# Optimization experiments

Measured on AMD Instinct MI355X. Metric: run time of the kernel, lower is better.

Reference implementation:

```python
import jax, jax.numpy as jnp
import numpy as np

QLEN, BSZ, D_MODEL = 2048, 4, 1024
N_HEAD, D_HEAD = 16, 64
SCALE = 1.0 / D_HEAD ** 0.5


def _rope(t, cos, sin):
    # t: [len, b, n, d_head]; cos/sin: [len, d_head//2]
    tr = t.reshape(*t.shape[:-1], D_HEAD // 2, 2)
    t_r, t_i = tr[..., 0], tr[..., 1]
    c = cos[:, None, None, :]
    s = sin[:, None, None, :]
    o_r = t_r * c - t_i * s
    o_i = t_r * s + t_i * c
    return jnp.stack([o_r, o_i], axis=-1).reshape(t.shape)


def setup_inputs() -> dict:
    key = jax.random.key(0)
    ks = jax.random.split(key, 9)
    x = jax.random.normal(ks[0], (QLEN, BSZ, D_MODEL), dtype=jnp.float32)
    # standard RoPE frequencies: theta = 10000^{-2i/d_head}
    inv_freq = 1.0 / (10000.0 ** (np.arange(0, D_HEAD, 2, dtype=np.float32) / D_HEAD))
    ang = np.arange(QLEN, dtype=np.float32)[:, None] * inv_freq[None, :]
    freqs_cos = jnp.asarray(np.cos(ang))
    freqs_sin = jnp.asarray(np.sin(ang))
    init = lambda k, sh: (jax.random.normal(k, sh, dtype=jnp.float32) * 0.02)
    H = N_HEAD * D_HEAD
    return {
        "x": x,
        "freqs_cos": freqs_cos,
        "freqs_sin": freqs_sin,
        "Wq": init(ks[1], (D_MODEL, H)), "bq": jnp.zeros((H,), jnp.float32),
        "Wk": init(ks[2], (D_MODEL, H)), "bk": jnp.zeros((H,), jnp.float32),
        "Wv": init(ks[3], (D_MODEL, H)), "bv": jnp.zeros((H,), jnp.float32),
        "Wo": init(ks[4], (H, D_MODEL)), "bo": jnp.zeros((D_MODEL,), jnp.float32),
    }


def reference(x, freqs_cos, freqs_sin, Wq, bq, Wk, bk, Wv, bv, Wo, bo):
    qlen, bsz, _ = x.shape
    q = x @ Wq + bq  # [q, b, n*d]
    k = x @ Wk + bk
    v = x @ Wv + bv
    new_mem = (k, v)
    q = q.reshape(qlen, bsz, N_HEAD, D_HEAD)
    k = k.reshape(qlen, bsz, N_HEAD, D_HEAD)
    vv = v.reshape(qlen, bsz, N_HEAD, D_HEAD)
    q = _rope(q, freqs_cos, freqs_sin)
    k = _rope(k, freqs_cos, freqs_sin)
    attn = jnp.einsum('ibnd,jbnd->ijbn', q, k) * SCALE
    p = jax.nn.softmax(attn, axis=1)
    o = jnp.einsum('ijbn,jbnd->ibnd', p, vv)
    o = o.reshape(qlen, bsz, N_HEAD * D_HEAD) @ Wo + bo
    return (o, new_mem[0], new_mem[1])
```

## Files before the change

### kernel.cpp

```cpp
#include <hip/hip_runtime.h>

typedef __attribute__((ext_vector_type(4))) float f32x4;
typedef __attribute__((ext_vector_type(16))) float f32x16;
typedef __attribute__((ext_vector_type(8))) __bf16 bf16x8;
typedef __attribute__((ext_vector_type(4))) __bf16 bf16x4;
typedef __attribute__((ext_vector_type(2))) __bf16 bf16x2;
typedef __attribute__((ext_vector_type(4))) unsigned int u32x4;

#define DEVI __device__ __forceinline__

static constexpr int QLEN = 2048, BSZ = 4, DM = 1024, NH = 16, DH = 64;
static constexpr int MROWS = QLEN * BSZ;
static constexpr long OSZ  = (long)MROWS * DM;
static constexpr float SCL2E = 0.125f * 1.4426950408889634f;
static constexpr float RAW_THR = 4.0f / SCL2E;

DEVI void gload_lds16(const void* g, void* l) {
  __builtin_amdgcn_global_load_lds(
      (__attribute__((address_space(1))) void*)(size_t)g,
      (__attribute__((address_space(3))) void*)l, 16, 0, 0);
}

DEVI f32x16 zero16() {
  f32x16 v;
#pragma unroll
  for (int i = 0; i < 16; ++i) v[i] = 0.f;
  return v;
}

DEVI unsigned pack_bf16(float lo, float hi) {
  bf16x2 v = { (__bf16)lo, (__bf16)hi };
  return __builtin_bit_cast(unsigned, v);
}

__global__ void k_f32_to_bf16(const float* __restrict__ in, __bf16* __restrict__ out, int n4) {
  int i = blockIdx.x * blockDim.x + threadIdx.x;
  int stride = gridDim.x * blockDim.x;
  for (; i < n4; i += stride) {
    const float4 v = ((const float4*)in)[i];
    bf16x4 o = { (__bf16)v.x, (__bf16)v.y, (__bf16)v.z, (__bf16)v.w };
    ((bf16x4*)out)[i] = o;
  }
}

__global__ void k_wtrans(const float* __restrict__ W, __bf16* __restrict__ Wt) {
  __shared__ float tile[64][65];
  const int tk = blockIdx.x >> 4;
  const int tn = blockIdx.x & 15;
  const int t = threadIdx.x;
  const int r = t >> 4;
  const int c4 = (t & 15) << 2;
#pragma unroll
  for (int i = 0; i < 4; ++i) {
    const float4 v = *(const float4*)&W[(size_t)(tk * 64 + r + i * 16) * DM + tn * 64 + c4];
    tile[r + i * 16][c4 + 0] = v.x;
    tile[r + i * 16][c4 + 1] = v.y;
    tile[r + i * 16][c4 + 2] = v.z;
    tile[r + i * 16][c4 + 3] = v.w;
  }
  __syncthreads();
#pragma unroll
  for (int i = 0; i < 4; ++i) {
    const int n = r + i * 16;
    bf16x4 o = { (__bf16)tile[c4 + 0][n], (__bf16)tile[c4 + 1][n],
                 (__bf16)tile[c4 + 2][n], (__bf16)tile[c4 + 3][n] };
    *(bf16x4*)&Wt[(size_t)(tn * 64 + n) * DM + tk * 64 + c4] = o;
  }
}

__global__ __launch_bounds__(256, 4) void k_vtrans(const __bf16* __restrict__ vb,
                                                   __bf16* __restrict__ VT) {
  __shared__ __bf16 tile[128 * 72];
  const int t = threadIdx.x;
  const int bh = blockIdx.x >> 4;
  const int s0 = (blockIdx.x & 15) * 128;
  const int b = bh >> 4, h = bh & 15;

  {
    const int r = t >> 1, hh = t & 1;
    const __bf16* src = vb + (size_t)((s0 + r) * 4 + b) * DM + h * 64 + hh * 32;
    __bf16* dst = tile + r * 72 + hh * 32;
#pragma unroll
    for (int k = 0; k < 4; ++k)
      *(bf16x8*)(dst + k * 8) = *(const bf16x8*)(src + k * 8);
  }
  __syncthreads();

  const int l = t & 63;
  const int w = t >> 6;
  const int hf = l >> 5;
#pragma unroll
  for (int gi = 0; gi < 4; ++gi) {
    const int idx = w * 4 + gi;
    const int ktl = idx >> 3;
    const int fi = idx & 7;
    const int jc = fi >> 1, dh = fi & 1;
    const int d = dh * 32 + (l & 31);
    const int j8 = ktl * 64 + jc * 16 + hf * 8;
    bf16x8 pk;
#pragma unroll
    for (int jj = 0; jj < 8; ++jj) pk[jj] = tile[(j8 + jj) * 72 + d];
    const int kt_g = (blockIdx.x & 15) * 2 + ktl;
    *(bf16x8*)&VT[(size_t)(((bh * 32 + kt_g) * 8 + fi) * 64 + l) * 8] = pk;
  }
}

DEVI void gemm_tile_core(const __bf16* __restrict__ A, const __bf16* __restrict__ Bt,
                         char* Alds, char* Blds, int m0, int n0, int t,
                         f32x4 (&acc)[4][4]) {
  constexpr int K = 1024;
  const int l = t & 63;
  const int w = t >> 6;
  const int wr = w >> 1, wc = w & 1;

  int a_addr[2][4], b_addr[2][4];
#pragma unroll
  for (int s = 0; s < 2; ++s)
#pragma unroll
    for (int f = 0; f < 4; ++f) {
      const int ca = s * 64 + ((l >> 4) << 4);
      const int ra = wr * 64 + f * 16 + (l & 15);
      a_addr[s][f] = ra * 128 + (ca ^ ((ra & 7) << 4));
      const int rb = wc * 64 + f * 16 + (l & 15);
      b_addr[s][f] = rb * 128 + (ca ^ ((rb & 7) << 4));
    }

  int g_row[4], g_col[4];
#pragma unroll
  for (int i = 0; i < 4; ++i) {
    const int g = i * 256 + t;
    g_row[i] = g >> 3;
    g_col[i] = ((g & 7) ^ (g_row[i] & 7)) * 8;
  }

  for (int kt = 0; kt < K / 64; ++kt) {
#pragma unroll
    for (int i = 0; i < 4; ++i) {
      gload_lds16(A + (size_t)(m0 + g_row[i]) * K + kt * 64 + g_col[i],
                  Alds + (size_t)(i * 256 + t) * 16);
      gload_lds16(Bt + (size_t)(n0 + g_row[i]) * K + kt * 64 + g_col[i],
                  Blds + (size_t)(i * 256 + t) * 16);
    }
    __syncthreads();
#pragma unroll
    for (int s = 0; s < 2; ++s) {
      bf16x8 af[4], bfr[4];
#pragma unroll
      for (int f = 0; f < 4; ++f) {
        af[f]  = *(const bf16x8*)(Alds + a_addr[s][f]);
        bfr[f] = *(const bf16x8*)(Blds + b_addr[s][f]);
      }
      __builtin_amdgcn_s_setprio(1);
#pragma unroll
      for (int mi = 0; mi < 4; ++mi)
#pragma unroll
        for (int ni = 0; ni < 4; ++ni)
          acc[mi][ni] = __builtin_amdgcn_mfma_f32_16x16x32_bf16(af[mi], bfr[ni], acc[mi][ni], 0, 0, 0);
      __builtin_amdgcn_s_setprio(0);
    }
    __syncthreads();
  }
}

__global__ __launch_bounds__(256, 2) void k_gemm(
    const __bf16* __restrict__ A, const __bf16* __restrict__ Bt,
    const float* __restrict__ bias, float* __restrict__ Cf) {
  __shared__ alignas(16) char lds[32768];
  const int t = threadIdx.x;
  const int l = t & 63;
  const int w = t >> 6;
  const int n0 = (blockIdx.x & 7) * 128;
  const int m0 = (blockIdx.x >> 3) * 128;
  const int wr = w >> 1, wc = w & 1;

  f32x4 acc[4][4];
#pragma unroll
  for (int i = 0; i < 4; ++i)
#pragma unroll
    for (int j = 0; j < 4; ++j) acc[i][j] = (f32x4){0.f, 0.f, 0.f, 0.f};

  gemm_tile_core(A, Bt, lds, lds + 16384, m0, n0, t, acc);

  const int rowb = m0 + wr * 64 + ((l >> 4) << 2);
  const int colb = n0 + wc * 64 + (l & 15);
#pragma unroll
  for (int ni = 0; ni < 4; ++ni) {
    const float bv = bias[colb + ni * 16];
#pragma unroll
    for (int mi = 0; mi < 4; ++mi)
#pragma unroll
      for (int r = 0; r < 4; ++r)
        Cf[(size_t)(rowb + mi * 16 + r) * 1024 + colb + ni * 16] = acc[mi][ni][r] + bv;
  }
}

__global__ __launch_bounds__(256, 2) void k_gemm_qkv(
    const __bf16* __restrict__ A, const __bf16* __restrict__ Bt,
    const float* __restrict__ bq, const float* __restrict__ bk, const float* __restrict__ bv,
    const float* __restrict__ fc, const float* __restrict__ fs,
    float* __restrict__ ok, float* __restrict__ ov,
    __bf16* __restrict__ qr, __bf16* __restrict__ kr, __bf16* __restrict__ vb) {
  __shared__ alignas(16) char lds[32768];
  const int t = threadIdx.x;
  const int l = t & 63;
  const int w = t >> 6;
  const int nt = blockIdx.x % 24;
  const int n0 = nt * 128;
  const int m0 = (blockIdx.x / 24) * 128;
  const int wr = w >> 1, wc = w & 1;

  f32x4 acc[4][4];
#pragma unroll
  for (int i = 0; i < 4; ++i)
#pragma unroll
    for (int j = 0; j < 4; ++j) acc[i][j] = (f32x4){0.f, 0.f, 0.f, 0.f};

  gemm_tile_core(A, Bt, lds, lds + 16384, m0, n0, t, acc);

  const int grp = n0 >> 10;
  const int rowb = m0 + wr * 64 + ((l >> 4) << 2);
  const int colb = (n0 & 1023) + wc * 64 + (l & 15);

  if (grp == 2) {
#pragma unroll
    for (int ni = 0; ni < 4; ++ni) {
      const float bvv = bv[colb + ni * 16];
#pragma unroll
      for (int mi = 0; mi < 4; ++mi)
#pragma unroll
        for (int r = 0; r < 4; ++r) {
          const float v = acc[mi][ni][r] + bvv;
          const size_t idx = (size_t)(rowb + mi * 16 + r) * 1024 + colb + ni * 16;
          ov[idx] = v;
          vb[idx] = (__bf16)v;
        }
    }
  } else {
    const float* bias = grp == 0 ? bq : bk;
    __bf16* Rb = grp == 0 ? qr : kr;
    const float sgn = (l & 1) ? 1.f : -1.f;
#pragma unroll
    for (int ni = 0; ni < 4; ++ni) {
      const int col = colb + ni * 16;
      const float bvv = bias[col];
      const int p = (col & 63) >> 1;
#pragma unroll
      for (int mi = 0; mi < 4; ++mi) {
        const int s_idx = (rowb + mi * 16) >> 2;
        const float cv = fc[s_idx * 32 + p];
        const float sv = fs[s_idx * 32 + p] * sgn;
#pragma unroll
        for (int r = 0; r < 4; ++r) {
          const float v = acc[mi][ni][r] + bvv;
          if (grp == 1) ok[(size_t)(rowb + mi * 16 + r) * 1024 + col] = v;
          const float part = __shfl_xor(v, 1);
          Rb[(size_t)(rowb + mi * 16 + r) * 1024 + col] = (__bf16)(v * cv + part * sv);
        }
      }
    }
  }
}

static constexpr int FBUF5 = 16384;

__global__ __launch_bounds__(256, 4) void k_flash5(
    const __bf16* __restrict__ Q, const __bf16* __restrict__ Kr,
    const __bf16* __restrict__ VT, __bf16* __restrict__ O) {
  __shared__ alignas(16) char lds[2 * FBUF5];

  const int t = threadIdx.x, l = t & 63, w = t >> 6;
  const int hf = l >> 5;
  const int q32 = l & 31;
  const int swz = (blockIdx.x & 7) * 128 + (blockIdx.x >> 3);
  const int qt = swz & 15;
  const int bh = swz >> 4;
  const int b = bh >> 4, hd = bh & 15;

  const int qrow = qt * 128 + w * 32 + q32;

  bf16x8 qf[4];
#pragma unroll
  for (int kc = 0; kc < 4; ++kc)
    qf[kc] = *(const bf16x8*)(Q + (size_t)(qrow * 4 + b) * DM + hd * 64 + kc * 16 + hf * 8);

  f32x16 acc0 = zero16(), acc1 = zero16();
  float m_run = -3.0e38f, l_run = 0.f;

  const int ksrc_j = t & 31;
  const int ksrc_d = (t >> 5) * 8;

#pragma unroll
  for (int i = 0; i < 2; ++i) {
    gload_lds16(Kr + (size_t)((i * 32 + ksrc_j) * 4 + b) * DM + hd * 64 + ksrc_d,
                lds + (size_t)(i * 256 + t) * 16);
    gload_lds16(VT + ((size_t)(bh * 32 + 0) * 512 + i * 256 + t) * 8,
                lds + 8192 + (size_t)(i * 256 + t) * 16);
  }

  for (int kt = 0; kt < QLEN / 64; ++kt) {
    const int cur = kt & 1;
    char* Kl = lds + cur * FBUF5;
    char* Vl = Kl + 8192;
    char* Kn = lds + (cur ^ 1) * FBUF5;
    char* Vn = Kn + 8192;

    __syncthreads();

    if (kt + 1 < QLEN / 64) {
#pragma unroll
      for (int i = 0; i < 2; ++i) {
        gload_lds16(Kr + (size_t)((((kt + 1) * 64) + i * 32 + ksrc_j) * 4 + b) * DM + hd * 64 + ksrc_d,
                    Kn + (size_t)(i * 256 + t) * 16);
        gload_lds16(VT + ((size_t)(bh * 32 + kt + 1) * 512 + i * 256 + t) * 8,
                    Vn + (size_t)(i * 256 + t) * 16);
      }
    }

    f32x16 s0 = zero16(), s1 = zero16();
    __builtin_amdgcn_s_setprio(1);
#pragma unroll
    for (int kc = 0; kc < 4; ++kc) {
      const bf16x8 kf0 = *(const bf16x8*)(Kl + (0 * 4 + kc) * 1024 + l * 16);
      const bf16x8 kf1 = *(const bf16x8*)(Kl + (1 * 4 + kc) * 1024 + l * 16);
      s0 = __builtin_amdgcn_mfma_f32_32x32x16_bf16(kf0, qf[kc], s0, 0, 0, 0);
      s1 = __builtin_amdgcn_mfma_f32_32x32x16_bf16(kf1, qf[kc], s1, 0, 0, 0);
    }
    __builtin_amdgcn_s_setprio(0);

    float r8[8];
#pragma unroll
    for (int i = 0; i < 8; ++i)
      r8[i] = fmaxf(fmaxf(s0[i], s0[i + 8]), fmaxf(s1[i], s1[i + 8]));
#pragma unroll
    for (int i = 0; i < 4; ++i) r8[i] = fmaxf(r8[i], r8[i + 4]);
    float pmax = fmaxf(fmaxf(r8[0], r8[1]), fmaxf(r8[2], r8[3]));
    pmax = fmaxf(pmax, __shfl_xor(pmax, 32));

    if (!__all(pmax - m_run <= RAW_THR)) {
      const float mn = fmaxf(m_run, pmax);
      const float alpha = __builtin_amdgcn_exp2f((m_run - mn) * SCL2E);
      l_run *= alpha;
      acc0 = acc0 * alpha;
      acc1 = acc1 * alpha;
      m_run = mn;
    }

#pragma unroll
    for (int r = 0; r < 16; ++r) {
      s0[r] = __builtin_amdgcn_exp2f((s0[r] - m_run) * SCL2E);
      s1[r] = __builtin_amdgcn_exp2f((s1[r] - m_run) * SCL2E);
    }
    float q8[8];
#pragma unroll
    for (int i = 0; i < 8; ++i) q8[i] = (s0[i] + s0[i + 8]) + (s1[i] + s1[i + 8]);
#pragma unroll
    for (int i = 0; i < 4; ++i) q8[i] = q8[i] + q8[i + 4];
    float rs = (q8[0] + q8[1]) + (q8[2] + q8[3]);
    rs += __shfl_xor(rs, 32);
    l_run += rs;

    unsigned pk[16];
#pragma unroll
    for (int m = 0; m < 4; ++m)
#pragma unroll
      for (int i = 0; i < 2; ++i) {
        pk[m * 2 + i]     = pack_bf16(s0[4 * m + 2 * i], s0[4 * m + 2 * i + 1]);
        pk[8 + m * 2 + i] = pack_bf16(s1[4 * m + 2 * i], s1[4 * m + 2 * i + 1]);
      }

#pragma unroll
    for (int c = 0; c < 2; ++c)
#pragma unroll
      for (int jc2 = 0; jc2 < 2; ++jc2) {
        unsigned w0 = pk[c * 8 + 4 * jc2 + 0], w2 = pk[c * 8 + 4 * jc2 + 2];
        unsigned w1 = pk[c * 8 + 4 * jc2 + 1], w3 = pk[c * 8 + 4 * jc2 + 3];
        asm("v_permlane32_swap_b32 %0, %1" : "+v"(w0), "+v"(w2));
        asm("v_permlane32_swap_b32 %0, %1" : "+v"(w1), "+v"(w3));
        const u32x4 pw = { w0, w1, w2, w3 };
        const bf16x8 pf = __builtin_bit_cast(bf16x8, pw);
        const int jc = c * 2 + jc2;
        const bf16x8 vf0 = *(const bf16x8*)(Vl + (jc * 2 + 0) * 1024 + l * 16);
        const bf16x8 vf1 = *(const bf16x8*)(Vl + (jc * 2 + 1) * 1024 + l * 16);
        __builtin_amdgcn_s_setprio(1);
        acc0 = __builtin_amdgcn_mfma_f32_32x32x16_bf16(vf0, pf, acc0, 0, 0, 0);
        acc1 = __builtin_amdgcn_mfma_f32_32x32x16_bf16(vf1, pf, acc1, 0, 0, 0);
        __builtin_amdgcn_s_setprio(0);
      }
  }

  const float inv = 1.0f / l_run;
#pragma unroll
  for (int g = 0; g < 4; ++g) {
    {
      const int d0 = 8 * g + 4 * hf;
      bf16x4 o4 = { (__bf16)(acc0[4 * g + 0] * inv), (__bf16)(acc0[4 * g + 1] * inv),
                    (__bf16)(acc0[4 * g + 2] * inv), (__bf16)(acc0[4 * g + 3] * inv) };
      *(bf16x4*)&O[(size_t)(qrow * 4 + b) * DM + hd * 64 + d0] = o4;
    }
    {
      const int d0 = 32 + 8 * g + 4 * hf;
      bf16x4 o4 = { (__bf16)(acc1[4 * g + 0] * inv), (__bf16)(acc1[4 * g + 1] * inv),
                    (__bf16)(acc1[4 * g + 2] * inv), (__bf16)(acc1[4 * g + 3] * inv) };
      *(bf16x4*)&O[(size_t)(qrow * 4 + b) * DM + hd * 64 + d0] = o4;
    }
  }
}

extern "C" void kernel_launch(void* const* d_in, const int* in_sizes, int n_in,
                              void* d_out, int out_size, void* d_ws, size_t ws_size,
                              hipStream_t stream) {
  const float* x    = (const float*)d_in[0];
  const float* fcos = (const float*)d_in[1];
  const float* fsin = (const float*)d_in[2];
  const float* Wq   = (const float*)d_in[3];
  const float* bq   = (const float*)d_in[4];
  const float* Wk   = (const float*)d_in[5];
  const float* bk   = (const float*)d_in[6];
  const float* Wv   = (const float*)d_in[7];
  const float* bv   = (const float*)d_in[8];
  const float* Wo   = (const float*)d_in[9];
  const float* bo   = (const float*)d_in[10];

  float* out_o = (float*)d_out;
  float* out_k = out_o + OSZ;
  float* out_v = out_o + 2 * OSZ;

  char* ws = (char*)d_ws;
  __bf16* xb  = (__bf16*)(ws);
  __bf16* VT  = (__bf16*)(ws);
  __bf16* wqt = (__bf16*)(ws + 16777216);
  __bf16* wkt = (__bf16*)(ws + 18874368);
  __bf16* wvt = (__bf16*)(ws + 20971520);
  __bf16* wot = (__bf16*)(ws + 23068672);
  __bf16* qr  = (__bf16*)(ws + 25165824);
  __bf16* kr  = (__bf16*)(ws + 41943040);
  __bf16* vb  = (__bf16*)(ws + 58720256);
  __bf16* ao  = (__bf16*)(ws + 75497472);

  k_f32_to_bf16<<<2048, 256, 0, stream>>>(x, xb, (int)(OSZ / 4));
  k_wtrans<<<256, 256, 0, stream>>>(Wq, wqt);
  k_wtrans<<<256, 256, 0, stream>>>(Wk, wkt);
  k_wtrans<<<256, 256, 0, stream>>>(Wv, wvt);
  k_wtrans<<<256, 256, 0, stream>>>(Wo, wot);

  k_gemm_qkv<<<1536, 256, 0, stream>>>(xb, wqt, bq, bk, bv, fcos, fsin,
                                       out_k, out_v, qr, kr, vb);

  k_vtrans<<<1024, 256, 0, stream>>>(vb, VT);

  k_flash5<<<1024, 256, 0, stream>>>(qr, kr, VT, ao);

  k_gemm<<<512, 256, 0, stream>>>(ao, wot, bo, out_o);
}
```

Before: 222.1 us.

## Merge weight transposes, raise GEMM occupancy, unroll flash double-buffer loop

Combines the four weight-transpose launches into a single launch that picks the source matrix from the block index. Raises the GEMM launch bounds from 2 to 3 blocks per CU, which lets the compiler target higher occupancy at the cost of fewer registers. Rewrites the flash attention loop as an explicitly unrolled ping-pong over two fixed LDS buffers, with incrementing pointers replacing per-iteration address arithmetic and buffer selection. Together these aim to cut launch overhead, improve latency hiding, and reduce loop overhead. The lower register budget could cause spills.

```diff
diff --git a/kernel.cpp b/kernel.cpp
--- a/kernel.cpp
+++ b/kernel.cpp
@@ -43,10 +43,16 @@
   }
 }
 
-__global__ void k_wtrans(const float* __restrict__ W, __bf16* __restrict__ Wt) {
+__global__ void k_wtrans4(const float* __restrict__ W0, const float* __restrict__ W1,
+                          const float* __restrict__ W2, const float* __restrict__ W3,
+                          __bf16* __restrict__ WtAll) {
   __shared__ float tile[64][65];
-  const int tk = blockIdx.x >> 4;
-  const int tn = blockIdx.x & 15;
+  const int g = blockIdx.x >> 8;
+  const float* W = g == 0 ? W0 : (g == 1 ? W1 : (g == 2 ? W2 : W3));
+  __bf16* Wt = WtAll + (size_t)g * DM * DM;
+  const int bid = blockIdx.x & 255;
+  const int tk = bid >> 4;
+  const int tn = bid & 15;
   const int t = threadIdx.x;
   const int r = t >> 4;
   const int c4 = (t & 15) << 2;
@@ -162,7 +168,7 @@
   }
 }
 
-__global__ __launch_bounds__(256, 2) void k_gemm(
+__global__ __launch_bounds__(256, 3) void k_gemm(
     const __bf16* __restrict__ A, const __bf16* __restrict__ Bt,
     const float* __restrict__ bias, float* __restrict__ Cf) {
   __shared__ alignas(16) char lds[32768];
@@ -194,7 +200,7 @@
   }
 }
 
-__global__ __launch_bounds__(256, 2) void k_gemm_qkv(
+__global__ __launch_bounds__(256, 3) void k_gemm_qkv(
     const __bf16* __restrict__ A, const __bf16* __restrict__ Bt,
     const float* __restrict__ bq, const float* __restrict__ bk, const float* __restrict__ bv,
     const float* __restrict__ fc, const float* __restrict__ fs,
@@ -261,12 +267,12 @@
   }
 }
 
-static constexpr int FBUF5 = 16384;
-
-__global__ __launch_bounds__(256, 4) void k_flash5(
+static constexpr int FBUF6 = 16384;
+
+__global__ __launch_bounds__(256, 4) void k_flash6(
     const __bf16* __restrict__ Q, const __bf16* __restrict__ Kr,
     const __bf16* __restrict__ VT, __bf16* __restrict__ O) {
-  __shared__ alignas(16) char lds[2 * FBUF5];
+  __shared__ alignas(16) char lds[2 * FBUF6];
 
   const int t = threadIdx.x, l = t & 63, w = t >> 6;
   const int hf = l >> 5;
@@ -286,36 +292,29 @@
   f32x16 acc0 = zero16(), acc1 = zero16();
   float m_run = -3.0e38f, l_run = 0.f;
 
-  const int ksrc_j = t & 31;
-  const int ksrc_d = (t >> 5) * 8;
-
-#pragma unroll
-  for (int i = 0; i < 2; ++i) {
-    gload_lds16(Kr + (size_t)((i * 32 + ksrc_j) * 4 + b) * DM + hd * 64 + ksrc_d,
-                lds + (size_t)(i * 256 + t) * 16);
-    gload_lds16(VT + ((size_t)(bh * 32 + 0) * 512 + i * 256 + t) * 8,
-                lds + 8192 + (size_t)(i * 256 + t) * 16);
-  }
-
-  for (int kt = 0; kt < QLEN / 64; ++kt) {
-    const int cur = kt & 1;
-    char* Kl = lds + cur * FBUF5;
-    char* Vl = Kl + 8192;
-    char* Kn = lds + (cur ^ 1) * FBUF5;
-    char* Vn = Kn + 8192;
-
-    __syncthreads();
-
-    if (kt + 1 < QLEN / 64) {
-#pragma unroll
-      for (int i = 0; i < 2; ++i) {
-        gload_lds16(Kr + (size_t)((((kt + 1) * 64) + i * 32 + ksrc_j) * 4 + b) * DM + hd * 64 + ksrc_d,
-                    Kn + (size_t)(i * 256 + t) * 16);
-        gload_lds16(VT + ((size_t)(bh * 32 + kt + 1) * 512 + i * 256 + t) * 8,
-                    Vn + (size_t)(i * 256 + t) * 16);
-      }
-    }
-
+  const size_t KSTRIDE = (size_t)64 * 4 * DM;
+  const size_t VSTRIDE = (size_t)512 * 8;
+  const __bf16* kp0 = Kr + (size_t)((t & 31) * 4 + b) * DM + hd * 64 + (t >> 5) * 8;
+  const __bf16* kp1 = kp0 + (size_t)32 * 4 * DM;
+  const __bf16* vp0 = VT + ((size_t)(bh * 32) * 512 + t) * 8;
+  const __bf16* vp1 = vp0 + 256 * 8;
+
+  char* const K0 = lds;
+  char* const V0 = lds + 8192;
+  char* const K1 = lds + FBUF6;
+  char* const V1 = K1 + 8192;
+
+#define STAGE6(Kn, Vn)                          \
+  do {                                          \
+    gload_lds16(kp0, (Kn) + t * 16);            \
+    gload_lds16(kp1, (Kn) + 4096 + t * 16);     \
+    gload_lds16(vp0, (Vn) + t * 16);            \
+    gload_lds16(vp1, (Vn) + 4096 + t * 16);     \
+    kp0 += KSTRIDE; kp1 += KSTRIDE;             \
+    vp0 += VSTRIDE; vp1 += VSTRIDE;             \
+  } while (0)
+
+  auto PROCESS = [&](const char* Kl, const char* Vl) {
     f32x16 s0 = zero16(), s1 = zero16();
     __builtin_amdgcn_s_setprio(1);
 #pragma unroll
@@ -386,7 +385,19 @@
         acc1 = __builtin_amdgcn_mfma_f32_32x32x16_bf16(vf1, pf, acc1, 0, 0, 0);
         __builtin_amdgcn_s_setprio(0);
       }
-  }
+  };
+
+  STAGE6(K0, V0);
+
+  for (int kt = 0; kt < QLEN / 64; kt += 2) {
+    __syncthreads();
+    STAGE6(K1, V1);
+    PROCESS(K0, V0);
+    __syncthreads();
+    if (kt + 2 < QLEN / 64) STAGE6(K0, V0);
+    PROCESS(K1, V1);
+  }
+#undef STAGE6
 
   const float inv = 1.0f / l_run;
 #pragma unroll
@@ -429,8 +440,6 @@
   __bf16* xb  = (__bf16*)(ws);
   __bf16* VT  = (__bf16*)(ws);
   __bf16* wqt = (__bf16*)(ws + 16777216);
-  __bf16* wkt = (__bf16*)(ws + 18874368);
-  __bf16* wvt = (__bf16*)(ws + 20971520);
   __bf16* wot = (__bf16*)(ws + 23068672);
   __bf16* qr  = (__bf16*)(ws + 25165824);
   __bf16* kr  = (__bf16*)(ws + 41943040);
@@ -438,17 +447,14 @@
   __bf16* ao  = (__bf16*)(ws + 75497472);
 
   k_f32_to_bf16<<<2048, 256, 0, stream>>>(x, xb, (int)(OSZ / 4));
-  k_wtrans<<<256, 256, 0, stream>>>(Wq, wqt);
-  k_wtrans<<<256, 256, 0, stream>>>(Wk, wkt);
-  k_wtrans<<<256, 256, 0, stream>>>(Wv, wvt);
-  k_wtrans<<<256, 256, 0, stream>>>(Wo, wot);
+  k_wtrans4<<<1024, 256, 0, stream>>>(Wq, Wk, Wv, Wo, wqt);
 
   k_gemm_qkv<<<1536, 256, 0, stream>>>(xb, wqt, bq, bk, bv, fcos, fsin,
                                        out_k, out_v, qr, kr, vb);
 
   k_vtrans<<<1024, 256, 0, stream>>>(vb, VT);
 
-  k_flash5<<<1024, 256, 0, stream>>>(qr, kr, VT, ao);
+  k_flash6<<<1024, 256, 0, stream>>>(qr, kr, VT, ao);
 
   k_gemm<<<512, 256, 0, stream>>>(ao, wot, bo, out_o);
 }
```

Result: faster. 216.1 us (-2.7%).
